# Optimization experiments

Hardware: AMD Instinct MI355X
Metric: run time of the kernel (lower is better)

The kernel has to match this reference:

```python
import jax, jax.numpy as jnp
import numpy as np

N_HEAD = 16
HEAD_SIZE = 64
N_EMBD = 1024
B, T = 4, 2048
THETA = 10000.0


def _rope_cos_sin(t_len, dim):
    # freqs: (dim//2,), angles: (T, dim//2)
    inv = 1.0 / (THETA ** (jnp.arange(0, dim, 2, dtype=jnp.float32) / dim))
    ang = jnp.arange(t_len, dtype=jnp.float32)[:, None] * inv[None, :]
    return jnp.cos(ang), jnp.sin(ang)


def _apply_rope(x, cos, sin):
    # x: (B, H, T, hs) -> complex-pair rotation over last dim
    xr = x.reshape(*x.shape[:-1], -1, 2)
    x0, x1 = xr[..., 0], xr[..., 1]
    c = cos[None, None, :, :]
    s = sin[None, None, :, :]
    o0 = x0 * c - x1 * s
    o1 = x0 * s + x1 * c
    return jnp.stack([o0, o1], axis=-1).reshape(x.shape)


def setup_inputs() -> dict:
    key = jax.random.key(0)
    ks = jax.random.split(key, 5)
    scale = 1.0 / np.sqrt(N_EMBD)
    return {
        "x": jax.random.normal(ks[0], (B, T, N_EMBD), dtype=jnp.float32),
        "Wq": jax.random.normal(ks[1], (N_EMBD, N_HEAD * HEAD_SIZE), dtype=jnp.float32) * scale,
        "Wk": jax.random.normal(ks[2], (N_EMBD, N_HEAD * HEAD_SIZE), dtype=jnp.float32) * scale,
        "Wv": jax.random.normal(ks[3], (N_EMBD, N_HEAD * HEAD_SIZE), dtype=jnp.float32) * scale,
        "Wp": jax.random.normal(ks[4], (N_HEAD * HEAD_SIZE, N_EMBD), dtype=jnp.float32) * scale,
        "bp": jnp.zeros((N_EMBD,), dtype=jnp.float32),
    }


def reference(x, Wq, Wk, Wv, Wp, bp):
    Bx, Tx, C = x.shape
    q = (x @ Wq).reshape(Bx, Tx, N_HEAD, HEAD_SIZE).transpose(0, 2, 1, 3)
    k = (x @ Wk).reshape(Bx, Tx, N_HEAD, HEAD_SIZE).transpose(0, 2, 1, 3)
    v = (x @ Wv).reshape(Bx, Tx, N_HEAD, HEAD_SIZE).transpose(0, 2, 1, 3)
    cos, sin = _rope_cos_sin(Tx, HEAD_SIZE)
    q = _apply_rope(q, cos, sin)
    k = _apply_rope(k, cos, sin)
    wei = jnp.einsum('bhqd,bhkd->bhqk', q, k) * (HEAD_SIZE ** -0.5)
    causal = jnp.tril(jnp.ones((Tx, Tx), dtype=bool))
    wei = jnp.where(causal[None, None, :, :], wei, -jnp.inf)
    wei = jax.nn.softmax(wei, axis=-1)
    out = jnp.einsum('bhqk,bhkd->bhqd', wei, v)
    out = out.transpose(0, 2, 1, 3).reshape(Bx, Tx, N_HEAD * HEAD_SIZE)
    return out @ Wp + bp
```

## Files before the change

### kernel.cpp

```cpp
#include <hip/hip_runtime.h>
#include <hip/hip_bf16.h>

#define NH 16
#define HS 64
#define CE 1024
#define BB 4
#define TT 2048

typedef __bf16 bf16;
typedef __bf16 v8bf __attribute__((ext_vector_type(8)));
typedef __bf16 v4bf __attribute__((ext_vector_type(4)));
typedef __bf16 v2bf __attribute__((ext_vector_type(2)));
typedef float v4f __attribute__((ext_vector_type(4)));
typedef float v16f __attribute__((ext_vector_type(16)));

#define GLD16(gp, lp)                                                              \
    __builtin_amdgcn_global_load_lds((const __attribute__((address_space(1))) void*)(gp), \
                                     (__attribute__((address_space(3))) void*)(lp), 16, 0, 0)

#define FENCE() __builtin_amdgcn_sched_barrier(0)
#define BARRIER() { FENCE(); __builtin_amdgcn_s_barrier(); FENCE(); }
#define VM4()  { asm volatile("s_waitcnt vmcnt(4)" ::: "memory"); FENCE(); }
#define VM8()  { asm volatile("s_waitcnt vmcnt(8)" ::: "memory"); FENCE(); }
#define VM0()  { asm volatile("s_waitcnt vmcnt(0)" ::: "memory"); FENCE(); }

__global__ __launch_bounds__(256) void prep_kernel(const float* __restrict__ x,
                                                   const float* __restrict__ W0,
                                                   const float* __restrict__ W1,
                                                   const float* __restrict__ W2,
                                                   const float* __restrict__ W3,
                                                   bf16* __restrict__ xb,
                                                   float2* __restrict__ csQ,
                                                   float2* __restrict__ csK,
                                                   bf16* __restrict__ dqkv,
                                                   bf16* __restrict__ dp) {
    __shared__ bf16 tile[64][66];
    const int bid = blockIdx.x;
    const int tid = threadIdx.x;
    if (bid < 4096) {
        int idx = (bid * 256 + tid) * 8;
        const float4* xp = (const float4*)(x + idx);
        float4 a = xp[0], b = xp[1];
        v8bf o;
        o[0] = (bf16)a.x; o[1] = (bf16)a.y; o[2] = (bf16)a.z; o[3] = (bf16)a.w;
        o[4] = (bf16)b.x; o[5] = (bf16)b.y; o[6] = (bf16)b.z; o[7] = (bf16)b.w;
        *(v8bf*)(xb + idx) = o;
    } else if (bid < 4352) {
        int idx = (bid - 4096) * 256 + tid;
        int t = idx >> 5, i = idx & 31;
        float inv = exp2f(-0.41524101186092034f * (float)i);
        float ang = (float)t * inv;
        float s, c;
        sincosf(ang, &s, &c);
        const float QS = 0.18033688011112042f;
        csK[idx] = make_float2(c, s);
        csQ[idx] = make_float2(c * QS, s * QS);
    } else {
        int idx = bid - 4352;
        int z = idx >> 8, rem = idx & 255;
        const float* W = (z == 0) ? W0 : (z == 1) ? W1 : (z == 2) ? W2 : W3;
        bf16* Wt = (z < 3) ? (dqkv + (size_t)z * 1024 * CE) : dp;
        int k0 = (rem & 15) * 64;
        int n0 = (rem >> 4) * 64;
        int tx = tid & 63;
        int ty = tid >> 6;
        for (int s = 0; s < 16; s++) {
            int r = s * 4 + ty;
            tile[r][tx] = (bf16)W[(size_t)(k0 + r) * CE + n0 + tx];
        }
        __syncthreads();
        for (int s = 0; s < 16; s++) {
            int r = s * 4 + ty;
            Wt[(size_t)(n0 + r) * CE + k0 + tx] = tile[tx][r];
        }
    }
}

#define GSTAGE(AD, BD, kk) {                                                        \
    _Pragma("unroll") for (int p = 0; p < 4; p++)                                   \
        GLD16(Ag + (kk) + (size_t)(p * 32) * CE, (AD) + p * 2048);                  \
    _Pragma("unroll") for (int p = 0; p < 4; p++)                                   \
        GLD16(Bg + (kk) + (size_t)(p * 32) * CE, (BD) + p * 2048); }

#define GCOMPUTE(ASrc, BSrc)                                                        \
    _Pragma("unroll")                                                               \
    for (int kh = 0; kh < 2; kh++) {                                                \
        v8bf af[4], bfr[4];                                                         \
        for (int i = 0; i < 4; i++) {                                               \
            int row = wr * 64 + i * 16 + lane15;                                    \
            af[i] = *(const v8bf*)(&ASrc[row * 64 + (((kh * 4 + quad) ^ (lane15 & 7)) * 8)]); \
        }                                                                           \
        for (int j = 0; j < 4; j++) {                                               \
            int row = wc * 64 + j * 16 + lane15;                                    \
            bfr[j] = *(const v8bf*)(&BSrc[row * 64 + (((kh * 4 + quad) ^ (lane15 & 7)) * 8)]); \
        }                                                                           \
        for (int i = 0; i < 4; i++)                                                 \
            for (int j = 0; j < 4; j++)                                             \
                acc[i][j] = __builtin_amdgcn_mfma_f32_16x16x32_bf16(af[i], bfr[j], acc[i][j], 0, 0, 0); \
    }

template <int MODE>
__global__ __launch_bounds__(256) void gemm_bt(const bf16* __restrict__ A,
                                               const bf16* __restrict__ Bt,
                                               bf16* __restrict__ Qb_, bf16* __restrict__ Kb_,
                                               bf16* __restrict__ Vt_,
                                               float* __restrict__ Pout,
                                               const float* __restrict__ bias,
                                               const float2* __restrict__ csQ,
                                               const float2* __restrict__ csK) {
    __shared__ __align__(16) bf16 As0[128 * 64];
    __shared__ __align__(16) bf16 Bs0[128 * 64];
    __shared__ __align__(16) bf16 As1[128 * 64];
    __shared__ __align__(16) bf16 Bs1[128 * 64];
    const int tid = threadIdx.x;
    const int lane = tid & 63, wave = tid >> 6;
    const int lane15 = lane & 15, quad = lane >> 4;
    const int wr = wave >> 1, wc = wave & 1;
    const int m0 = blockIdx.y * 128;
    const int n0 = blockIdx.x * 128;

    v4f acc[4][4] = {};

    const int cm = tid >> 3;
    const int ck = ((tid & 7) ^ (cm & 7)) * 8;
    const bf16* Ag = A + (size_t)(m0 + cm) * CE + ck;
    const bf16* Bg = Bt + (size_t)(n0 + cm) * CE + ck;
    bf16* aD0 = &As0[wave * 512];
    bf16* bD0 = &Bs0[wave * 512];
    bf16* aD1 = &As1[wave * 512];
    bf16* bD1 = &Bs1[wave * 512];

    GSTAGE(aD0, bD0, 0);
    for (int k0 = 0; k0 < CE; k0 += 128) {
        GSTAGE(aD1, bD1, k0 + 64);
        VM8(); BARRIER();
        GCOMPUTE(As0, Bs0);
        BARRIER();
        GSTAGE(aD0, bD0, (k0 + 128) & 1023);
        VM8(); BARRIER();
        GCOMPUTE(As1, Bs1);
        BARRIER();
    }
    VM0();

    for (int i = 0; i < 4; i++) {
        for (int j = 0; j < 4; j++) {
            int gmb = m0 + wr * 64 + i * 16 + quad * 4;
            int gn = n0 + wc * 64 + j * 16 + lane15;
            if (MODE == 1) {
                float bb = bias[gn];
                for (int r = 0; r < 4; r++)
                    Pout[(size_t)(gmb + r) * CE + gn] = acc[i][j][r] + bb;
            } else {
                int w = gn >> 10;
                int n = gn & 1023;
                int hh = n >> 6, d = n & 63;
                if (w < 2) {
                    bf16* out = w ? Kb_ : Qb_;
                    const float2* csRow = (w ? csK : csQ) + (d >> 1);
                    for (int r = 0; r < 4; r++) {
                        int gm = gmb + r;
                        int b = gm >> 11, t = gm & 2047;
                        float xv = acc[i][j][r];
                        float pv = __shfl_xor(xv, 1);
                        float2 cs = csRow[t * 32];
                        float ov = (gn & 1) ? (pv * cs.y + xv * cs.x)
                                            : (xv * cs.x - pv * cs.y);
                        out[(((size_t)(b * NH + hh)) * TT + t) * HS + d] = (bf16)ov;
                    }
                } else {
                    int b = gmb >> 11, t = gmb & 2047;
                    v4bf pack;
                    for (int r = 0; r < 4; r++) pack[r] = (bf16)acc[i][j][r];
                    *(v4bf*)(&Vt_[(((size_t)(b * NH + hh)) * HS + d) * TT + t]) = pack;
                }
            }
        }
    }
}

#define ASTAGE(KD, VD, kv) {                                        \
    GLD16(kg + (size_t)(kv) * HS, (KD));                            \
    GLD16(kg + (size_t)((kv) + 32) * HS, (KD) + 2048);              \
    GLD16(vg + (kv), (VD));                                         \
    GLD16(vg + (kv) + 32 * TT, (VD) + 2048); }

#define ACOMPUTE(KS, VS, KVB)                                                       \
    _Pragma("unroll")                                                               \
    for (int sub = 0; sub < 2; sub++) {                                             \
        const int kvs = (KVB) + sub * 32;                                           \
        if (kvs > q0) break;                                                        \
        const bool diag = (kvs == q0);                                              \
        v16f s = {};                                                                \
        for (int m = 0; m < 4; m++) {                                               \
            v8bf afr = *(const v8bf*)(&KS[(sub * 32 + lane31) * 64 +                \
                                          (((m << 1) | h) ^ (lane31 & 7)) * 8]);    \
            s = __builtin_amdgcn_mfma_f32_32x32x16_bf16(afr, qf[m], s, 0, 0, 0);    \
        }                                                                           \
        float p[16];                                                                \
        if (diag) {                                                                 \
            for (int r = 0; r < 16; r++) {                                          \
                int kvr = (r & 3) + 8 * (r >> 2) + 4 * h;                           \
                p[r] = exp2f((kvr <= lane31) ? s[r] : -3.0e38f);                    \
            }                                                                       \
        } else {                                                                    \
            for (int r = 0; r < 16; r++) p[r] = exp2f(s[r]);                        \
        }                                                                           \
        float a8[8];                                                                \
        for (int r = 0; r < 8; r++) a8[r] = p[r] + p[r + 8];                        \
        l_i += ((a8[0] + a8[1]) + (a8[2] + a8[3])) + ((a8[4] + a8[5]) + (a8[6] + a8[7])); \
        union { v4bf v; unsigned long long u; } ch[4];                              \
        for (int g = 0; g < 4; g++)                                                 \
            for (int rr = 0; rr < 4; rr++)                                          \
                ch[g].v[rr] = (bf16)p[g * 4 + rr];                                  \
        for (int t2 = 0; t2 < 2; t2++) {                                            \
            unsigned long long mine0 = ch[2 * t2].u, mine1 = ch[2 * t2 + 1].u;      \
            unsigned long long send = h ? mine0 : mine1;                            \
            unsigned long long recv = __shfl_xor(send, 32);                         \
            union { v8bf v; unsigned long long u[2]; } bfr2;                        \
            bfr2.u[0] = h ? recv : mine0;                                           \
            bfr2.u[1] = h ? mine1 : recv;                                           \
            int cidx = (((sub << 2) + (t2 << 1) + h) ^ (lane31 & 7)) * 8;           \
            v8bf va0 = *(const v8bf*)(&VS[lane31 * 64 + cidx]);                     \
            o0 = __builtin_amdgcn_mfma_f32_32x32x16_bf16(va0, bfr2.v, o0, 0, 0, 0); \
            v8bf va1 = *(const v8bf*)(&VS[(32 + lane31) * 64 + cidx]);              \
            o1 = __builtin_amdgcn_mfma_f32_32x32x16_bf16(va1, bfr2.v, o1, 0, 0, 0); \
        }                                                                           \
    }

__global__ __launch_bounds__(256, 4) void attn_kernel(const bf16* __restrict__ Qb,
                                                      const bf16* __restrict__ Kb,
                                                      const bf16* __restrict__ Vt,
                                                      bf16* __restrict__ Ob) {
    __shared__ __align__(16) bf16 Ks0[64 * 64];
    __shared__ __align__(16) bf16 Vs0[64 * 64];
    __shared__ __align__(16) bf16 Ks1[64 * 64];
    __shared__ __align__(16) bf16 Vs1[64 * 64];
    const int tid = threadIdx.x, lane = tid & 63, wave = tid >> 6;
    const int lane31 = lane & 31, h = lane >> 5;
    const int bh = blockIdx.x & 63;
    const int qb = 15 - (int)(blockIdx.x >> 6);
    const int q0 = qb * 128 + wave * 32;
    const bf16* Qp = Qb + (size_t)bh * TT * HS;
    const bf16* Kp = Kb + (size_t)bh * TT * HS;
    const bf16* Vp = Vt + (size_t)bh * HS * TT;

    v8bf qf[4];
    for (int m = 0; m < 4; m++)
        qf[m] = *(const v8bf*)(Qp + (size_t)(q0 + lane31) * HS + m * 16 + h * 8);

    v16f o0 = {}, o1 = {};
    float l_i = 0.f;

    const int kr = tid >> 3, kc = tid & 7;
    const bf16* kg = Kp + kr * HS + ((kc ^ (kr & 7)) * 8);
    const bf16* vg = Vp + (size_t)kr * TT + ((kc ^ (kr & 7)) * 8);
    bf16* ksD0 = &Ks0[wave * 512];
    bf16* vsD0 = &Vs0[wave * 512];
    bf16* ksD1 = &Ks1[wave * 512];
    bf16* vsD1 = &Vs1[wave * 512];

    const int kv_max = qb * 128 + 96;
    ASTAGE(ksD0, vsD0, 0);
    for (int kv0 = 0; kv0 <= kv_max; kv0 += 128) {
        ASTAGE(ksD1, vsD1, kv0 + 64);
        VM4(); BARRIER();
        ACOMPUTE(Ks0, Vs0, kv0);
        BARRIER();
        ASTAGE(ksD0, vsD0, (kv0 + 128) & 2047);
        VM4(); BARRIER();
        ACOMPUTE(Ks1, Vs1, kv0 + 64);
        BARRIER();
    }
    VM0();

    const int b = bh >> 4, hh = bh & 15;
    const int q = q0 + lane31;
    float lt = l_i + __shfl_xor(l_i, 32);
    float invl = 1.f / lt;
    bf16* outRow = Ob + ((size_t)(b * TT + q)) * CE + hh * HS;
    for (int g = 0; g < 4; g++) {
        v4bf w0, w1;
        for (int rr = 0; rr < 4; rr++) {
            w0[rr] = (bf16)(o0[g * 4 + rr] * invl);
            w1[rr] = (bf16)(o1[g * 4 + rr] * invl);
        }
        *(v4bf*)(outRow + g * 8 + h * 4) = w0;
        *(v4bf*)(outRow + 32 + g * 8 + h * 4) = w1;
    }
}

extern "C" void kernel_launch(void* const* d_in, const int* in_sizes, int n_in,
                              void* d_out, int out_size, void* d_ws, size_t ws_size,
                              hipStream_t stream) {
    const float* x  = (const float*)d_in[0];
    const float* Wq = (const float*)d_in[1];
    const float* Wk = (const float*)d_in[2];
    const float* Wv = (const float*)d_in[3];
    const float* Wp = (const float*)d_in[4];
    const float* bp = (const float*)d_in[5];
    char* ws = (char*)d_ws;
    const size_t MB = 1024 * 1024;
    bf16* Xb    = (bf16*)(ws);
    bf16* WqkvT = (bf16*)(ws + 16 * MB);
    bf16* WpT   = (bf16*)(ws + 22 * MB);
    bf16* Qb    = (bf16*)(ws + 24 * MB);
    bf16* Kb    = (bf16*)(ws + 40 * MB);
    bf16* Vt    = (bf16*)(ws + 56 * MB);
    bf16* Ob    = (bf16*)(ws + 72 * MB);
    float2* csQ = (float2*)(ws + 72 * MB);
    float2* csK = (float2*)(ws + 72 * MB + 512 * 1024);

    prep_kernel<<<dim3(5376), dim3(256), 0, stream>>>(x, Wq, Wk, Wv, Wp, Xb, csQ, csK,
                                                      WqkvT, WpT);

    gemm_bt<0><<<dim3(24, 64), dim3(256), 0, stream>>>(Xb, WqkvT, Qb, Kb, Vt, nullptr, nullptr,
                                                       csQ, csK);

    attn_kernel<<<dim3(1024), dim3(256), 0, stream>>>(Qb, Kb, Vt, Ob);

    gemm_bt<1><<<dim3(8, 64), dim3(256), 0, stream>>>(Ob, WpT, nullptr, nullptr, nullptr,
                                                      (float*)d_out, bp, nullptr, nullptr);
}
```

Before: 257.0 us.

## Pack RoPE epilogue into paired bf16 stores and raise wave priority around MFMAs

The QK projection epilogue now has each lane handle one complete rotated pair for two rows. It writes them as 2-element bf16 vector stores instead of four scalar stores per lane, which cuts store instruction count and improves coalescing. The attention inner loop also wraps its MFMA sections in s_setprio so waves issuing matrix work are favoured over others. The epilogue rewrite changes which lane handles which row and needs the shuffle and parity logic to stay correct.

```diff
diff --git a/kernel.cpp b/kernel.cpp
--- a/kernel.cpp
+++ b/kernel.cpp
@@ -158,16 +158,28 @@
                 if (w < 2) {
                     bf16* out = w ? Kb_ : Qb_;
                     const float2* csRow = (w ? csK : csQ) + (d >> 1);
-                    for (int r = 0; r < 4; r++) {
-                        int gm = gmb + r;
-                        int b = gm >> 11, t = gm & 2047;
-                        float xv = acc[i][j][r];
-                        float pv = __shfl_xor(xv, 1);
-                        float2 cs = csRow[t * 32];
-                        float ov = (gn & 1) ? (pv * cs.y + xv * cs.x)
-                                            : (xv * cs.x - pv * cs.y);
-                        out[(((size_t)(b * NH + hh)) * TT + t) * HS + d] = (bf16)ov;
-                    }
+                    const int par = gn & 1;
+                    const int dbase = d & ~1;
+                    const int b = gmb >> 11, tbase = gmb & 2047;
+                    const float xv0 = acc[i][j][0], xv1 = acc[i][j][1];
+                    const float xv2 = acc[i][j][2], xv3 = acc[i][j][3];
+                    const float pv0 = __shfl_xor(xv0, 1), pv1 = __shfl_xor(xv1, 1);
+                    const float pv2 = __shfl_xor(xv2, 1), pv3 = __shfl_xor(xv3, 1);
+                    const float xa = par ? xv2 : xv0, pa = par ? pv2 : pv0;
+                    const float xb2 = par ? xv3 : xv1, pb = par ? pv3 : pv1;
+                    const float ua = par ? pa : xa, va = par ? xa : pa;
+                    const float ub = par ? pb : xb2, vb = par ? xb2 : pb;
+                    const int ta = tbase + (par << 1), tb = ta + 1;
+                    const float2 csa = csRow[ta * 32];
+                    const float2 csb = csRow[tb * 32];
+                    v2bf sa, sb;
+                    sa[0] = (bf16)(ua * csa.x - va * csa.y);
+                    sa[1] = (bf16)(ua * csa.y + va * csa.x);
+                    sb[0] = (bf16)(ub * csb.x - vb * csb.y);
+                    sb[1] = (bf16)(ub * csb.y + vb * csb.x);
+                    bf16* rowp = out + ((size_t)(b * NH + hh)) * TT * HS + dbase;
+                    *(v2bf*)(rowp + (size_t)ta * HS) = sa;
+                    *(v2bf*)(rowp + (size_t)tb * HS) = sb;
                 } else {
                     int b = gmb >> 11, t = gmb & 2047;
                     v4bf pack;
@@ -192,11 +204,13 @@
         if (kvs > q0) break;                                                        \
         const bool diag = (kvs == q0);                                              \
         v16f s = {};                                                                \
+        __builtin_amdgcn_s_setprio(1);                                              \
         for (int m = 0; m < 4; m++) {                                               \
             v8bf afr = *(const v8bf*)(&KS[(sub * 32 + lane31) * 64 +                \
                                           (((m << 1) | h) ^ (lane31 & 7)) * 8]);    \
             s = __builtin_amdgcn_mfma_f32_32x32x16_bf16(afr, qf[m], s, 0, 0, 0);    \
         }                                                                           \
+        __builtin_amdgcn_s_setprio(0);                                              \
         float p[16];                                                                \
         if (diag) {                                                                 \
             for (int r = 0; r < 16; r++) {                                          \
@@ -213,6 +227,7 @@
         for (int g = 0; g < 4; g++)                                                 \
             for (int rr = 0; rr < 4; rr++)                                          \
                 ch[g].v[rr] = (bf16)p[g * 4 + rr];                                  \
+        __builtin_amdgcn_s_setprio(1);                                              \
         for (int t2 = 0; t2 < 2; t2++) {                                            \
             unsigned long long mine0 = ch[2 * t2].u, mine1 = ch[2 * t2 + 1].u;      \
             unsigned long long send = h ? mine0 : mine1;                            \
@@ -226,6 +241,7 @@
             v8bf va1 = *(const v8bf*)(&VS[(32 + lane31) * 64 + cidx]);              \
             o1 = __builtin_amdgcn_mfma_f32_32x32x16_bf16(va1, bfr2.v, o1, 0, 0, 0); \
         }                                                                           \
+        __builtin_amdgcn_s_setprio(0);                                              \
     }
 
 __global__ __launch_bounds__(256, 4) void attn_kernel(const bf16* __restrict__ Qb,
```

New measurement: 256.2 us. No clear change (-0.3%).
